# Kernel optimization log

Measured on AMD Instinct MI355X. Metric: run time of the kernel, lower is better.

## Reference

```python
import jax, jax.numpy as jnp
import numpy as np
from jax import lax

B, C, H, W, D = 2, 64, 32, 32, 32
N = H * W * D          # input_size = 32768
P = 64                 # proj_size
NH = 4                 # num_heads
HD = C // NH           # head dim = 16
LN_EPS = 1e-5
BN_EPS = 1e-5


def setup_inputs() -> dict:
    key = jax.random.key(0)
    ks = jax.random.split(key, 10)
    s = lambda k, shape: (jax.random.normal(k, shape, jnp.float32) * 0.02)
    return dict(
        x=jax.random.normal(ks[0], (B, C, H, W, D), jnp.float32),
        ln_w=jnp.ones((C,), jnp.float32), ln_b=jnp.zeros((C,), jnp.float32),
        gamma=1e-6 * jnp.ones((C,), jnp.float32),
        temp1=jnp.ones((NH, 1, 1), jnp.float32),
        temp2=jnp.ones((NH, 1, 1), jnp.float32),
        W_qkvv=s(ks[1], (4 * C, C)),                      # Linear(C,4C), no bias
        W_EF=s(ks[2], (P, N)), b_EF=jnp.zeros((P,), jnp.float32),  # shared E=F
        W_o1=s(ks[3], (C // 2, C)), b_o1=jnp.zeros((C // 2,), jnp.float32),
        W_o2=s(ks[4], (C // 2, C)), b_o2=jnp.zeros((C // 2,), jnp.float32),
        conv1_w=s(ks[5], (C, C, 3, 3, 3)),
        conv2_w=s(ks[6], (C, C, 3, 3, 3)),
        bn1_w=jnp.ones((C,), jnp.float32), bn1_b=jnp.zeros((C,), jnp.float32),
        bn2_w=jnp.ones((C,), jnp.float32), bn2_b=jnp.zeros((C,), jnp.float32),
        conv8_w=s(ks[7], (C, C, 1, 1, 1)), conv8_b=jnp.zeros((C,), jnp.float32),
    )


def _ln(x, w, b):
    mu = jnp.mean(x, axis=-1, keepdims=True)
    var = jnp.mean(jnp.square(x - mu), axis=-1, keepdims=True)
    return (x - mu) * lax.rsqrt(var + LN_EPS) * w + b


def _l2norm(x):  # F.normalize(dim=-1), eps=1e-12
    n = jnp.sqrt(jnp.sum(jnp.square(x), axis=-1, keepdims=True))
    return x / jnp.maximum(n, 1e-12)


def _bn_eval(x, w, b):  # BatchNorm3d in eval mode, running mean 0 / var 1
    scale = (w * lax.rsqrt(jnp.float32(1.0 + BN_EPS))).reshape(1, -1, 1, 1, 1)
    return x * scale + b.reshape(1, -1, 1, 1, 1)


def _conv3d(x, w, pad):
    return lax.conv_general_dilated(
        x, w, window_strides=(1, 1, 1), padding=[(pad, pad)] * 3,
        dimension_numbers=('NCDHW', 'OIDHW', 'NCDHW'))


def _lrelu(x):
    return jnp.where(x >= 0, x, 0.01 * x)


def _epa(xn, W_qkvv, W_EF, b_EF, temp1, temp2, W_o1, b_o1, W_o2, b_o2):
    b, n, c = xn.shape
    qkvv = (xn @ W_qkvv.T).reshape(b, n, 4, NH, HD).transpose(2, 0, 3, 1, 4)  # [4,B,h,N,d]
    q, k, v_ca, v_sa = [jnp.swapaxes(qkvv[i], -2, -1) for i in range(4)]      # [B,h,d,N]
    # shared linear projection E = F over the token axis N -> P
    k_proj = jnp.einsum('bhdn,pn->bhdp', k, W_EF) + b_EF
    v_proj = jnp.einsum('bhdn,pn->bhdp', v_sa, W_EF) + b_EF
    qn, kn = _l2norm(q), _l2norm(k)
    # channel attention: [B,h,d,d]
    attn_ca = jax.nn.softmax(jnp.einsum('bhdn,bhen->bhde', qn, kn) * temp1, axis=-1)
    x_ca = jnp.einsum('bhde,bhen->bhdn', attn_ca, v_ca)                       # [B,h,d,N]
    x_ca = x_ca.transpose(0, 3, 1, 2).reshape(b, n, c)
    # spatial attention with projected K/V: [B,h,N,P]
    attn_sa = jax.nn.softmax(jnp.einsum('bhdn,bhdp->bhnp', qn, k_proj) * temp2, axis=-1)
    x_sa = jnp.einsum('bhnp,bhdp->bhnd', attn_sa, v_proj)                     # [B,h,N,d]
    # faithful to original UNETR++ code: permute(0,3,1,2) then reshape(B,N,C)
    x_sa = x_sa.transpose(0, 3, 1, 2).reshape(b, n, c)
    x_sa = x_sa @ W_o1.T + b_o1
    x_ca = x_ca @ W_o2.T + b_o2
    return jnp.concatenate([x_sa, x_ca], axis=-1)


def reference(x, ln_w, ln_b, gamma, temp1, temp2, W_qkvv, W_EF, b_EF,
              W_o1, b_o1, W_o2, b_o2, conv1_w, conv2_w,
              bn1_w, bn1_b, bn2_w, bn2_b, conv8_w, conv8_b):
    b, c, h, w, d = x.shape
    xs = x.reshape(b, c, h * w * d).transpose(0, 2, 1)  # [B,N,C]
    attn = xs + gamma * _epa(_ln(xs, ln_w, ln_b), W_qkvv, W_EF, b_EF,
                             temp1, temp2, W_o1, b_o1, W_o2, b_o2)
    attn_skip = attn.reshape(b, h, w, d, c).transpose(0, 4, 1, 2, 3)  # [B,C,H,W,D]
    # UnetResBlock (stride 1, in==out -> identity residual), BN in eval mode
    out = _lrelu(_bn_eval(_conv3d(attn_skip, conv1_w, 1), bn1_w, bn1_b))
    out = _bn_eval(_conv3d(out, conv2_w, 1), bn2_w, bn2_b)
    out = _lrelu(out + attn_skip)
    # conv8: Dropout3d (off, eval) + 1x1x1 conv with bias
    y = _conv3d(out, conv8_w, 0) + conv8_b.reshape(1, -1, 1, 1, 1)
    return attn_skip + y
```

## Files before the change

kernel.cpp:

```cpp
#include <hip/hip_runtime.h>

#define NTOK 32768

typedef __attribute__((ext_vector_type(8))) short short8;
typedef __attribute__((ext_vector_type(4))) short short4_t;
typedef __attribute__((ext_vector_type(4))) float f32x4;

__device__ __forceinline__ short f2b(float f) {
    union { float f; unsigned u; } v; v.f = f;
    unsigned r = v.u + 0x7fffu + ((v.u >> 16) & 1u);
    return (short)(r >> 16);
}
__device__ __forceinline__ float b2f(short s) {
    union { float f; unsigned u; } v;
    v.u = ((unsigned)(unsigned short)s) << 16;
    return v.f;
}

__global__ void k_repack(const float* __restrict__ w1, const float* __restrict__ w2,
                         const float* __restrict__ w8, const float* __restrict__ wef,
                         const float* __restrict__ wq, const float* __restrict__ bEF,
                         short* __restrict__ wb1, short* __restrict__ wb2,
                         short* __restrict__ wb8, short* __restrict__ wefb,
                         short* __restrict__ wqb, float* __restrict__ kp,
                         float* __restrict__ vp, float* __restrict__ qd)
{
    int i = blockIdx.x * 256 + threadIdx.x;
    if (i >= 2349312) return;
    if (i >= 2347008) { qd[i - 2347008] = 0.f; return; }
    if (i >= 2338816) {
        int j = i - 2338816;
        float v = bEF[j & 63];
        kp[j] = v; vp[j] = v; return;
    }
    if (i >= 2322432) { int j = i - 2322432; wqb[j] = f2b(wq[j]); return; }
    if (i >= 225280)  { int j = i - 225280;  wefb[j] = f2b(wef[j]); return; }
    if (i >= 221184)  { int j = i - 221184;  wb8[j] = f2b(w8[j]); return; }
    int sel = i >= 110592;
    int j = sel ? i - 110592 : i;
    int tap = j >> 12;
    int r = j & 4095;
    int oc = r >> 6, ic = r & 63;
    const float* w = sel ? w2 : w1;
    short* o = sel ? wb2 : wb1;
    o[j] = f2b(w[(oc * 64 + ic) * 27 + tap]);
}

__global__ __launch_bounds__(256) void k_ln_qkvv(
    const float* __restrict__ x, const float* __restrict__ lnw,
    const float* __restrict__ lnb, const short* __restrict__ wqb,
    short* __restrict__ qkvvb)
{
    __shared__ __align__(16) short Wl[256 * 72];
    __shared__ __align__(16) short tr[256 * 72];
    __shared__ float red1[4][64], red2[4][64];
    __shared__ float mu_s[64], rs_s[64];
    short* al = tr;

    int bid = blockIdx.x;
    int b = bid >> 9;
    int n0 = (bid & 511) << 6;
    int tid = threadIdx.x;

    for (int i = tid; i < 2048; i += 256) {
        int out = i >> 3, q8 = (i & 7) * 8;
        *(short8*)&Wl[out * 72 + q8] = *(const short8*)&wqb[out * 64 + q8];
    }

    int t = tid & 63, cq = tid >> 6;
    float xr[16];
    float s1 = 0.f, s2 = 0.f;
    const float* xb = x + (((size_t)(b * 64 + cq * 16)) << 15) + n0 + t;
#pragma unroll
    for (int j = 0; j < 16; ++j) {
        float v = xb[(size_t)j << 15];
        xr[j] = v; s1 += v; s2 += v * v;
    }
    red1[cq][t] = s1; red2[cq][t] = s2;
    __syncthreads();
    if (tid < 64) {
        float a = red1[0][tid] + red1[1][tid] + red1[2][tid] + red1[3][tid];
        float q = red2[0][tid] + red2[1][tid] + red2[2][tid] + red2[3][tid];
        float mu = a * (1.f / 64.f);
        float var = q * (1.f / 64.f) - mu * mu;
        mu_s[tid] = mu;
        rs_s[tid] = rsqrtf(var + 1e-5f);
    }
    __syncthreads();
    {
        float mu = mu_s[t], rs = rs_s[t];
        short8 p0, p1;
#pragma unroll
        for (int j = 0; j < 8; ++j) {
            int c = cq * 16 + j;
            p0[j] = f2b((xr[j] - mu) * rs * lnw[c] + lnb[c]);
        }
#pragma unroll
        for (int j = 0; j < 8; ++j) {
            int c = cq * 16 + 8 + j;
            p1[j] = f2b((xr[8 + j] - mu) * rs * lnw[c] + lnb[c]);
        }
        *(short8*)&al[t * 72 + cq * 16] = p0;
        *(short8*)&al[t * 72 + cq * 16 + 8] = p1;
    }
    __syncthreads();

    int w = tid >> 6, lane = tid & 63, l15 = lane & 15, quad = lane >> 4;
    f32x4 acc[4][4];
#pragma unroll
    for (int mt = 0; mt < 4; ++mt)
#pragma unroll
        for (int nt = 0; nt < 4; ++nt) acc[mt][nt] = (f32x4){0.f, 0.f, 0.f, 0.f};
#pragma unroll
    for (int ks = 0; ks < 2; ++ks) {
        short8 af[4], bf[4];
#pragma unroll
        for (int mt = 0; mt < 4; ++mt)
            af[mt] = *(const short8*)&al[(mt * 16 + l15) * 72 + quad * 8 + ks * 32];
#pragma unroll
        for (int nt = 0; nt < 4; ++nt)
            bf[nt] = *(const short8*)&Wl[(w * 64 + nt * 16 + l15) * 72 + quad * 8 + ks * 32];
#pragma unroll
        for (int mt = 0; mt < 4; ++mt)
#pragma unroll
            for (int nt = 0; nt < 4; ++nt)
                acc[mt][nt] = __builtin_amdgcn_mfma_f32_16x16x32_bf16(af[mt], bf[nt], acc[mt][nt], 0, 0, 0);
    }
    __syncthreads();

#pragma unroll
    for (int mt = 0; mt < 4; ++mt)
#pragma unroll
        for (int nt = 0; nt < 4; ++nt) {
            int out = w * 64 + nt * 16 + l15;
            short4_t sv;
#pragma unroll
            for (int r = 0; r < 4; ++r) sv[r] = f2b(acc[mt][nt][r]);
            *(short4_t*)&tr[out * 72 + mt * 16 + quad * 4] = sv;
        }
    __syncthreads();
    for (int i = tid; i < 2048; i += 256) {
        int o = i >> 3, tq = (i & 7) * 8;
        short8 v = *(const short8*)&tr[o * 72 + tq];
        int isel = o >> 6, h = (o >> 4) & 3, d = o & 15;
        *(short8*)&qkvvb[((size_t)(((isel * 2 + b) * 4 + h) * 16 + d) << 15) + n0 + tq] = v;
    }
}

__global__ __launch_bounds__(256) void k_pq(
    const short* __restrict__ qkvvb, const short* __restrict__ wefb,
    float* __restrict__ kp, float* __restrict__ vp, float* __restrict__ qd,
    float* __restrict__ qn_acc, float* __restrict__ kn_acc)
{
    __shared__ float redb[3][64][38];
    int kc = blockIdx.x, bh = blockIdx.y;
    int tid = threadIdx.x;
    int w = tid >> 6, lane = tid & 63, l15 = lane & 15, quad = lane >> 4;
    size_t qrow = ((size_t)(bh * 16 + l15)) << 15;
    size_t krow = ((size_t)(128 + bh * 16 + l15)) << 15;
    size_t vrow = ((size_t)(384 + bh * 16 + l15)) << 15;
    int nbase = kc * 1024 + w * 256 + quad * 8;
    f32x4 acck[4], accv[4], accqd, accqq, acckk;
#pragma unroll
    for (int nt = 0; nt < 4; ++nt) {
        acck[nt] = (f32x4){0.f, 0.f, 0.f, 0.f};
        accv[nt] = (f32x4){0.f, 0.f, 0.f, 0.f};
    }
    accqd = (f32x4){0.f, 0.f, 0.f, 0.f};
    accqq = (f32x4){0.f, 0.f, 0.f, 0.f};
    acckk = (f32x4){0.f, 0.f, 0.f, 0.f};
#pragma unroll
    for (int ks = 0; ks < 8; ++ks) {
        int n = nbase + ks * 32;
        short8 qf = *(const short8*)&qkvvb[qrow + n];
        short8 kf = *(const short8*)&qkvvb[krow + n];
        short8 vf = *(const short8*)&qkvvb[vrow + n];
        accqd = __builtin_amdgcn_mfma_f32_16x16x32_bf16(qf, kf, accqd, 0, 0, 0);
        accqq = __builtin_amdgcn_mfma_f32_16x16x32_bf16(qf, qf, accqq, 0, 0, 0);
        acckk = __builtin_amdgcn_mfma_f32_16x16x32_bf16(kf, kf, acckk, 0, 0, 0);
#pragma unroll
        for (int nt = 0; nt < 4; ++nt) {
            short8 wf = *(const short8*)&wefb[(((size_t)(nt * 16 + l15)) << 15) + n];
            acck[nt] = __builtin_amdgcn_mfma_f32_16x16x32_bf16(kf, wf, acck[nt], 0, 0, 0);
            accv[nt] = __builtin_amdgcn_mfma_f32_16x16x32_bf16(vf, wf, accv[nt], 0, 0, 0);
        }
    }
    int diag = (quad == (l15 >> 2));
    float qqv = diag ? accqq[l15 & 3] : 0.f;
    float kkv = diag ? acckk[l15 & 3] : 0.f;
    if (w > 0) {
        float* p = &redb[w - 1][lane][0];
#pragma unroll
        for (int nt = 0; nt < 4; ++nt)
#pragma unroll
            for (int r = 0; r < 4; ++r) { p[nt * 4 + r] = acck[nt][r]; p[16 + nt * 4 + r] = accv[nt][r]; }
#pragma unroll
        for (int r = 0; r < 4; ++r) p[32 + r] = accqd[r];
        p[36] = qqv; p[37] = kkv;
    }
    __syncthreads();
    if (w == 0) {
#pragma unroll
        for (int wv = 0; wv < 3; ++wv) {
            const float* p = &redb[wv][lane][0];
#pragma unroll
            for (int nt = 0; nt < 4; ++nt)
#pragma unroll
                for (int r = 0; r < 4; ++r) { acck[nt][r] += p[nt * 4 + r]; accv[nt][r] += p[16 + nt * 4 + r]; }
#pragma unroll
            for (int r = 0; r < 4; ++r) accqd[r] += p[32 + r];
            qqv += p[36]; kkv += p[37];
        }
        int d = quad * 4;
#pragma unroll
        for (int nt = 0; nt < 4; ++nt)
#pragma unroll
            for (int r = 0; r < 4; ++r) {
                int idx = (bh * 16 + d + r) * 64 + nt * 16 + l15;
                atomicAdd(&kp[idx], acck[nt][r]);
                atomicAdd(&vp[idx], accv[nt][r]);
            }
#pragma unroll
        for (int r = 0; r < 4; ++r)
            atomicAdd(&qd[bh * 256 + (d + r) * 16 + l15], accqd[r]);
        if (diag) {
            atomicAdd(&qn_acc[bh * 16 + l15], qqv);
            atomicAdd(&kn_acc[bh * 16 + l15], kkv);
        }
    }
}

__global__ __launch_bounds__(256) void k_attn(
    const short* __restrict__ qkvvb, const float* __restrict__ qd,
    const float* __restrict__ qn_acc, const float* __restrict__ kn_acc,
    const float* __restrict__ temp1, const float* __restrict__ kp,
    const float* __restrict__ vp, const float* __restrict__ temp2,
    short* __restrict__ xsab, short* __restrict__ xcab)
{
    __shared__ float kl[16][68];
    __shared__ float vl[16][68];
    __shared__ float alca[16][17];
    __shared__ float iqs[16], iks[16];
    __shared__ __align__(16) short Pl[4][64][72];
    __shared__ short Ol[4][64][17];
    int bh = blockIdx.y; int b = bh >> 2, h = bh & 3;
    int tid = threadIdx.x;
    for (int i = tid; i < 1024; i += 256) {
        kl[i >> 6][i & 63] = kp[bh * 1024 + i];
        vl[i >> 6][i & 63] = vp[bh * 1024 + i];
    }
    if (tid < 32) {
        int j = tid & 15;
        float v = (tid < 16) ? qn_acc[bh * 16 + j] : kn_acc[bh * 16 + j];
        float rv = 1.f / fmaxf(sqrtf(v), 1e-12f);
        if (tid < 16) iqs[j] = rv; else iks[j] = rv;
    }
    __syncthreads();
    {
        int r = tid >> 4, e = tid & 15;
        float v = qd[bh * 256 + tid] * iqs[r] * iks[e] * temp1[h];
        float mx = v;
#pragma unroll
        for (int m = 1; m < 16; m <<= 1) mx = fmaxf(mx, __shfl_xor(mx, m));
        float ex = __expf(v - mx);
        float s = ex;
#pragma unroll
        for (int m = 1; m < 16; m <<= 1) s += __shfl_xor(s, m);
        alca[r][e] = ex / s;
    }
    __syncthreads();

    int w = tid >> 6, lane = tid & 63, l15 = lane & 15, quad = lane >> 4;
    int tw = (blockIdx.x << 8) + w * 64;
    float t2 = temp2[h];
    const short8 zero8 = {0, 0, 0, 0, 0, 0, 0, 0};
    int xs = (l15 & 7) << 3;

    short8 qb[4];
    if (quad < 2) {
#pragma unroll
        for (int tnt = 0; tnt < 4; ++tnt) {
            short8 v;
#pragma unroll
            for (int j = 0; j < 8; ++j) {
                int d = quad * 8 + j;
                short qv = qkvvb[(((size_t)(bh * 16 + d)) << 15) + tw + tnt * 16 + l15];
                v[j] = f2b(b2f(qv) * iqs[d]);
            }
            qb[tnt] = v;
        }
    } else {
#pragma unroll
        for (int tnt = 0; tnt < 4; ++tnt) qb[tnt] = zero8;
    }
    short8 ka[4];
    if (quad < 2) {
#pragma unroll
        for (int pmt = 0; pmt < 4; ++pmt) {
            short8 v;
#pragma unroll
            for (int j = 0; j < 8; ++j) v[j] = f2b(kl[quad * 8 + j][pmt * 16 + l15]);
            ka[pmt] = v;
        }
    } else {
#pragma unroll
        for (int pmt = 0; pmt < 4; ++pmt) ka[pmt] = zero8;
    }

    f32x4 st[4][4];
#pragma unroll
    for (int pmt = 0; pmt < 4; ++pmt)
#pragma unroll
        for (int tnt = 0; tnt < 4; ++tnt) st[pmt][tnt] = (f32x4){0.f, 0.f, 0.f, 0.f};
#pragma unroll
    for (int pmt = 0; pmt < 4; ++pmt)
#pragma unroll
        for (int tnt = 0; tnt < 4; ++tnt)
            st[pmt][tnt] = __builtin_amdgcn_mfma_f32_16x16x32_bf16(ka[pmt], qb[tnt], st[pmt][tnt], 0, 0, 0);

#pragma unroll
    for (int tnt = 0; tnt < 4; ++tnt) {
        int tok = tnt * 16 + l15;
        float v[16];
        float mx = -1e30f;
#pragma unroll
        for (int pmt = 0; pmt < 4; ++pmt)
#pragma unroll
            for (int r = 0; r < 4; ++r) {
                float x = st[pmt][tnt][r] * t2;
                v[pmt * 4 + r] = x; mx = fmaxf(mx, x);
            }
        mx = fmaxf(mx, __shfl_xor(mx, 16));
        mx = fmaxf(mx, __shfl_xor(mx, 32));
        float s = 0.f;
#pragma unroll
        for (int i2 = 0; i2 < 16; ++i2) { v[i2] = __expf(v[i2] - mx); s += v[i2]; }
        s += __shfl_xor(s, 16);
        s += __shfl_xor(s, 32);
        float inv = 1.f / s;
#pragma unroll
        for (int pmt = 0; pmt < 4; ++pmt)
#pragma unroll
            for (int t = 0; t < 2; ++t) {
                unsigned lo = (unsigned short)f2b(v[pmt * 4 + 2 * t] * inv);
                unsigned hi = (unsigned short)f2b(v[pmt * 4 + 2 * t + 1] * inv);
                int col = (pmt * 16 + quad * 4 + 2 * t) ^ xs;
                *(unsigned*)&Pl[w][tok][col] = lo | (hi << 16);
            }
    }

    short8 vb[2];
#pragma unroll
    for (int ks = 0; ks < 2; ++ks) {
        short8 t;
#pragma unroll
        for (int j = 0; j < 8; ++j) t[j] = f2b(vl[l15][quad * 8 + ks * 32 + j]);
        vb[ks] = t;
    }
    f32x4 vo[4];
#pragma unroll
    for (int mt = 0; mt < 4; ++mt) vo[mt] = (f32x4){0.f, 0.f, 0.f, 0.f};
#pragma unroll
    for (int mt = 0; mt < 4; ++mt) {
        int tok = mt * 16 + l15;
#pragma unroll
        for (int ks = 0; ks < 2; ++ks) {
            short8 pa = *(const short8*)&Pl[w][tok][(quad * 8 + ks * 32) ^ xs];
            vo[mt] = __builtin_amdgcn_mfma_f32_16x16x32_bf16(pa, vb[ks], vo[mt], 0, 0, 0);
        }
    }

    short8 ab[4], bb;
    if (quad < 2) {
        short8 t;
#pragma unroll
        for (int j = 0; j < 8; ++j) t[j] = f2b(alca[l15][quad * 8 + j]);
        bb = t;
#pragma unroll
        for (int mt = 0; mt < 4; ++mt) {
            short8 u;
#pragma unroll
            for (int j = 0; j < 8; ++j)
                u[j] = qkvvb[(((size_t)(256 + bh * 16 + quad * 8 + j)) << 15) + tw + mt * 16 + l15];
            ab[mt] = u;
        }
    } else {
        bb = zero8;
#pragma unroll
        for (int mt = 0; mt < 4; ++mt) ab[mt] = zero8;
    }
    f32x4 ca[4];
#pragma unroll
    for (int mt = 0; mt < 4; ++mt) ca[mt] = (f32x4){0.f, 0.f, 0.f, 0.f};
#pragma unroll
    for (int mt = 0; mt < 4; ++mt)
        ca[mt] = __builtin_amdgcn_mfma_f32_16x16x32_bf16(ab[mt], bb, ca[mt], 0, 0, 0);

#pragma unroll
    for (int mt = 0; mt < 4; ++mt)
#pragma unroll
        for (int r = 0; r < 4; ++r) {
            int tok = tw + mt * 16 + quad * 4 + r;
            xcab[((size_t)(b * NTOK + tok)) * 64 + h * 16 + l15] = f2b(ca[mt][r]);
        }

#pragma unroll
    for (int mt = 0; mt < 4; ++mt)
#pragma unroll
        for (int r = 0; r < 4; ++r)
            Ol[w][mt * 16 + quad * 4 + r][l15] = f2b(vo[mt][r]);
#pragma unroll
    for (int d = 0; d < 16; ++d) {
        short vv = Ol[w][lane][d];
        xsab[(size_t)b * 2097152 + (((size_t)(d * 4 + h)) << 15) + tw + lane] = vv;
    }
}

__global__ __launch_bounds__(256) void k_epilogue(
    const float* __restrict__ x, const short* __restrict__ xsab,
    const short* __restrict__ xcab, const float* __restrict__ Wo1,
    const float* __restrict__ bo1, const float* __restrict__ Wo2,
    const float* __restrict__ bo2, const float* __restrict__ gamma,
    float* __restrict__ attn_skip, short* __restrict__ gA)
{
    __shared__ __align__(16) short Wl[64 * 72];
    __shared__ __align__(16) short trS[256 * 72];
    int tid = threadIdx.x;
    int bidx = blockIdx.x;
    int b = bidx >> 7;
    int n0 = (bidx & 127) << 8;
    for (int i = tid; i < 4096; i += 256) {
        int row = i >> 6, c = i & 63;
        float wv = (row < 32) ? Wo1[row * 64 + c] : Wo2[(row - 32) * 64 + c];
        Wl[row * 72 + c] = f2b(wv);
    }
    __syncthreads();

    int w = tid >> 6, lane = tid & 63, l15 = lane & 15, quad = lane >> 4;
    int tw = n0 + w * 64;
    const short* sa_base = xsab + (size_t)b * 2097152;
    const short* ca_base = xcab + (size_t)b * 2097152;

    f32x4 acc_sa[4][2], acc_ca[4][2];
#pragma unroll
    for (int mt = 0; mt < 4; ++mt)
#pragma unroll
        for (int nt = 0; nt < 2; ++nt) {
            acc_sa[mt][nt] = (f32x4){0.f, 0.f, 0.f, 0.f};
            acc_ca[mt][nt] = (f32x4){0.f, 0.f, 0.f, 0.f};
        }
#pragma unroll
    for (int ks = 0; ks < 2; ++ks) {
        int ko = quad * 8 + ks * 32;
        short8 b1[2], b2[2];
#pragma unroll
        for (int nt = 0; nt < 2; ++nt) {
            b1[nt] = *(const short8*)&Wl[(nt * 16 + l15) * 72 + ko];
            b2[nt] = *(const short8*)&Wl[(32 + nt * 16 + l15) * 72 + ko];
        }
#pragma unroll
        for (int mt = 0; mt < 4; ++mt) {
            int trow = tw + mt * 16 + l15;
            short8 a1 = *(const short8*)&sa_base[(size_t)trow * 64 + ko];
            short8 a2 = *(const short8*)&ca_base[(size_t)trow * 64 + ko];
#pragma unroll
            for (int nt = 0; nt < 2; ++nt) {
                acc_sa[mt][nt] = __builtin_amdgcn_mfma_f32_16x16x32_bf16(a1, b1[nt], acc_sa[mt][nt], 0, 0, 0);
                acc_ca[mt][nt] = __builtin_amdgcn_mfma_f32_16x16x32_bf16(a2, b2[nt], acc_ca[mt][nt], 0, 0, 0);
            }
        }
    }

#pragma unroll
    for (int half = 0; half < 2; ++half) {
#pragma unroll
        for (int nt = 0; nt < 2; ++nt) {
            int c = half * 32 + nt * 16 + l15;
            float g = gamma[c];
            float bias = half ? bo2[c - 32] : bo1[c];
#pragma unroll
            for (int mt = 0; mt < 4; ++mt) {
                f32x4 a = half ? acc_ca[mt][nt] : acc_sa[mt][nt];
                int tbase = tw + mt * 16 + quad * 4;
                size_t gidx = (((size_t)(b * 64 + c)) << 15) + tbase;
                f32x4 xv = *(const f32x4*)&x[gidx];
                f32x4 o;
#pragma unroll
                for (int r = 0; r < 4; ++r) {
                    float v = xv[r] + g * (a[r] + bias);
                    o[r] = v;
                    trS[(w * 64 + mt * 16 + quad * 4 + r) * 72 + c] = f2b(v);
                }
                *(f32x4*)&attn_skip[gidx] = o;
            }
        }
    }
    __syncthreads();
    for (int i = tid; i < 2048; i += 256) {
        int tok = i >> 3, cq = (i & 7) * 8;
        short8 v = *(const short8*)&trS[tok * 72 + cq];
        *(short8*)&gA[((size_t)(b * NTOK + n0 + tok)) * 64 + cq] = v;
    }
}

template <int MODE>
__global__ __launch_bounds__(256) void k_conv3m(
    const short* __restrict__ gin, const short* __restrict__ wb,
    const float* __restrict__ bnw, const float* __restrict__ bnb,
    const float* __restrict__ skip, short* __restrict__ goutS,
    const short* __restrict__ wb8, const float* __restrict__ b8,
    float* __restrict__ io)
{
    __shared__ __align__(16) short inl_s[24480];
    __shared__ __align__(16) short wl_s[15360];
    int bx = blockIdx.x;
    int bb = bx >> 8;
    int z0 = (bx >> 3) & 31;
    int y0 = (bx & 7) * 4;
    int tid = threadIdx.x;
    int lane = tid & 63, wv = tid >> 6;
    int l15 = lane & 15, quad = lane >> 4;
    int wo = tid >> 2, wq = tid & 3;

    f32x4 acc[2][4];
#pragma unroll
    for (int s = 0; s < 2; ++s)
#pragma unroll
        for (int nt = 0; nt < 4; ++nt) acc[s][nt] = (f32x4){0.f, 0.f, 0.f, 0.f};

    for (int chunk = 0; chunk < 2; ++chunk) {
        const short* wck = wb + chunk * 32 + wq * 8;
        short8 wr[3];
#pragma unroll
        for (int t = 0; t < 3; ++t)
            wr[t] = *(const short8*)&wck[(size_t)(t * 64 + wo) * 64];
        __syncthreads();
        for (int i = tid; i < 2448; i += 256) {
            int p = i >> 2, icq = i & 3;
            int xi = p % 34; int t2 = p / 34; int yi = t2 % 6; int zi = t2 / 6;
            int gz = z0 + zi - 1, gy = y0 + yi - 1, gx = xi - 1;
            short8 v = {0, 0, 0, 0, 0, 0, 0, 0};
            if ((unsigned)gz < 32u && (unsigned)gy < 32u && (unsigned)gx < 32u)
                v = *(const short8*)&gin[((size_t)(bb * NTOK + gz * 1024 + gy * 32 + gx)) * 64 + chunk * 32 + icq * 8];
            *(short8*)&inl_s[p * 40 + icq * 8] = v;
        }
#pragma unroll
        for (int t = 0; t < 3; ++t)
            *(short8*)&wl_s[(t * 64 + wo) * 40 + wq * 8] = wr[t];

#pragma unroll
        for (int kz = 0; kz < 3; ++kz)
#pragma unroll
        for (int ky = 0; ky < 3; ++ky) {
            const int sidx = kz * 3 + ky;
            __syncthreads();
            if (sidx < 8) {
#pragma unroll
                for (int t = 0; t < 3; ++t)
                    wr[t] = *(const short8*)&wck[(size_t)(((sidx + 1) * 3 + t) * 64 + wo) * 64];
            }
            const short* wcur = &wl_s[(sidx & 1) * 7680];
            int rowb = (kz * 6 + wv + ky) * 34;
#pragma unroll
            for (int kx = 0; kx < 3; ++kx) {
                short8 bf[4];
#pragma unroll
                for (int nt = 0; nt < 4; ++nt)
                    bf[nt] = *(const short8*)&wcur[(kx * 64 + nt * 16 + l15) * 40 + quad * 8];
#pragma unroll
                for (int s = 0; s < 2; ++s) {
                    short8 af = *(const short8*)&inl_s[(rowb + s * 16 + l15 + kx) * 40 + quad * 8];
#pragma unroll
                    for (int nt = 0; nt < 4; ++nt)
                        acc[s][nt] = __builtin_amdgcn_mfma_f32_16x16x32_bf16(af, bf[nt], acc[s][nt], 0, 0, 0);
                }
            }
            if (sidx < 8) {
                short* wnext = &wl_s[((sidx + 1) & 1) * 7680];
#pragma unroll
                for (int t = 0; t < 3; ++t)
                    *(short8*)&wnext[(t * 64 + wo) * 40 + wq * 8] = wr[t];
            }
        }
    }
    __syncthreads();
    float rb = rsqrtf(1.f + 1e-5f);
    if (MODE == 0) {
        short* outS = inl_s;
#pragma unroll
        for (int nt = 0; nt < 4; ++nt) {
            int oc = nt * 16 + l15;
            float sc_ = bnw[oc] * rb, sh_ = bnb[oc];
#pragma unroll
            for (int s = 0; s < 2; ++s) {
                f32x4 v = acc[s][nt];
#pragma unroll
                for (int r = 0; r < 4; ++r) {
                    int pos = wv * 32 + s * 16 + quad * 4 + r;
                    float val = v[r] * sc_ + sh_;
                    val = val >= 0.f ? val : 0.01f * val;
                    outS[pos * 72 + oc] = f2b(val);
                }
            }
        }
        __syncthreads();
        for (int i = tid; i < 1024; i += 256) {
            int p = i >> 3, cq = i & 7;
            short8 v = *(const short8*)&outS[p * 72 + cq * 8];
            int y = p >> 5, x = p & 31;
            *(short8*)&goutS[((size_t)(bb * NTOK + z0 * 1024 + (y0 + y) * 32 + x)) * 64 + cq * 8] = v;
        }
    } else {
        float* outF = (float*)inl_s;
        short* a2_s = wl_s;
        short* w8_s = wl_s + 9216;
#pragma unroll
        for (int nt = 0; nt < 4; ++nt) {
            int oc = nt * 16 + l15;
#pragma unroll
            for (int s = 0; s < 2; ++s) {
                f32x4 v = acc[s][nt];
#pragma unroll
                for (int r = 0; r < 4; ++r) {
                    int pos = wv * 32 + s * 16 + quad * 4 + r;
                    outF[oc * 132 + pos] = v[r];
                }
            }
        }
        __syncthreads();
        f32x4 skr[8];
#pragma unroll
        for (int it = 0; it < 8; ++it) {
            int i = it * 256 + tid;
            int oc = i >> 5, xq = i & 31, pos0 = xq * 4;
            f32x4 c4 = *(const f32x4*)&outF[oc * 132 + pos0];
            int y = pos0 >> 5, xx = pos0 & 31;
            size_t g = (((size_t)(bb * 64 + oc)) << 15) + ((z0 * 32 + (y0 + y)) * 32 + xx);
            f32x4 sk = *(const f32x4*)&skip[g];
            skr[it] = sk;
            float sc_ = bnw[oc] * rb, sh_ = bnb[oc];
#pragma unroll
            for (int r = 0; r < 4; ++r) {
                float val = c4[r] * sc_ + sh_ + sk[r];
                val = val >= 0.f ? val : 0.01f * val;
                a2_s[(pos0 + r) * 72 + oc] = f2b(val);
            }
        }
        for (int i = tid; i < 512; i += 256) {
            int ocw = i >> 3, cq = i & 7;
            *(short8*)&w8_s[ocw * 80 + cq * 8] = *(const short8*)&wb8[ocw * 64 + cq * 8];
        }
        __syncthreads();
        f32x4 acc2[2][4];
#pragma unroll
        for (int s = 0; s < 2; ++s)
#pragma unroll
            for (int nt = 0; nt < 4; ++nt) acc2[s][nt] = (f32x4){0.f, 0.f, 0.f, 0.f};
#pragma unroll
        for (int ks = 0; ks < 2; ++ks) {
            short8 a8[2], b8f[4];
#pragma unroll
            for (int s = 0; s < 2; ++s)
                a8[s] = *(const short8*)&a2_s[(wv * 32 + s * 16 + l15) * 72 + quad * 8 + ks * 32];
#pragma unroll
            for (int nt = 0; nt < 4; ++nt)
                b8f[nt] = *(const short8*)&w8_s[(nt * 16 + l15) * 80 + quad * 8 + ks * 32];
#pragma unroll
            for (int s = 0; s < 2; ++s)
#pragma unroll
                for (int nt = 0; nt < 4; ++nt)
                    acc2[s][nt] = __builtin_amdgcn_mfma_f32_16x16x32_bf16(a8[s], b8f[nt], acc2[s][nt], 0, 0, 0);
        }
        __syncthreads();
#pragma unroll
        for (int nt = 0; nt < 4; ++nt) {
            int oc = nt * 16 + l15;
#pragma unroll
            for (int s = 0; s < 2; ++s) {
                f32x4 v = acc2[s][nt];
#pragma unroll
                for (int r = 0; r < 4; ++r) {
                    int pos = wv * 32 + s * 16 + quad * 4 + r;
                    outF[oc * 132 + pos] = v[r];
                }
            }
        }
        __syncthreads();
#pragma unroll
        for (int it = 0; it < 8; ++it) {
            int i = it * 256 + tid;
            int oc = i >> 5, xq = i & 31, pos0 = xq * 4;
            f32x4 cv = *(const f32x4*)&outF[oc * 132 + pos0];
            int y = pos0 >> 5, xx = pos0 & 31;
            size_t g = (((size_t)(bb * 64 + oc)) << 15) + ((z0 * 32 + (y0 + y)) * 32 + xx);
            float bias8 = b8[oc];
            f32x4 o;
#pragma unroll
            for (int r = 0; r < 4; ++r) o[r] = skr[it][r] + cv[r] + bias8;
            *(f32x4*)&io[g] = o;
        }
    }
}

extern "C" void kernel_launch(void* const* d_in, const int* in_sizes, int n_in,
                              void* d_out, int out_size, void* d_ws, size_t ws_size,
                              hipStream_t stream) {
    const float* x      = (const float*)d_in[0];
    const float* ln_w   = (const float*)d_in[1];
    const float* ln_b   = (const float*)d_in[2];
    const float* gamma  = (const float*)d_in[3];
    const float* temp1  = (const float*)d_in[4];
    const float* temp2  = (const float*)d_in[5];
    const float* W_qkvv = (const float*)d_in[6];
    const float* W_EF   = (const float*)d_in[7];
    const float* b_EF   = (const float*)d_in[8];
    const float* W_o1   = (const float*)d_in[9];
    const float* b_o1   = (const float*)d_in[10];
    const float* W_o2   = (const float*)d_in[11];
    const float* b_o2   = (const float*)d_in[12];
    const float* conv1w = (const float*)d_in[13];
    const float* conv2w = (const float*)d_in[14];
    const float* bn1_w  = (const float*)d_in[15];
    const float* bn1_b  = (const float*)d_in[16];
    const float* bn2_w  = (const float*)d_in[17];
    const float* bn2_b  = (const float*)d_in[18];
    const float* conv8w = (const float*)d_in[19];
    const float* conv8b = (const float*)d_in[20];

    short* qkvvb = (short*)d_ws;
    float* kp    = (float*)(qkvvb + 16777216);
    float* vp    = kp + 8192;
    float* qd    = vp + 8192;
    float* qn_acc= qd + 2048;
    float* kn_acc= qn_acc + 128;
    float* a_ca  = kn_acc + 128;
    float* iqn   = a_ca + 2048;
    float* ikn   = iqn + 128;
    short* xcab  = (short*)(ikn + 128);
    short* xsab  = xcab + 4194304;
    short* gA    = xsab + 4194304;
    short* g1    = gA + 4194304;
    short* wb1   = g1 + 4194304;
    short* wb2   = wb1 + 110592;
    short* wb8   = wb2 + 110592;
    short* wefb  = wb8 + 4096;
    short* wqb   = wefb + 2097152;

    float* attn_skip = (float*)d_out;

    hipLaunchKernelGGL(k_repack, dim3(9177), dim3(256), 0, stream,
                       conv1w, conv2w, conv8w, W_EF, W_qkvv, b_EF,
                       wb1, wb2, wb8, wefb, wqb, kp, vp, qd);
    hipLaunchKernelGGL(k_ln_qkvv, dim3(1024), dim3(256), 0, stream,
                       x, ln_w, ln_b, wqb, qkvvb);
    hipLaunchKernelGGL(k_pq, dim3(32, 8), dim3(256), 0, stream,
                       qkvvb, wefb, kp, vp, qd, qn_acc, kn_acc);
    hipLaunchKernelGGL(k_attn, dim3(128, 8), dim3(256), 0, stream,
                       qkvvb, qd, qn_acc, kn_acc, temp1, kp, vp, temp2, xsab, xcab);
    hipLaunchKernelGGL(k_epilogue, dim3(256), dim3(256), 0, stream,
                       x, xsab, xcab, W_o1, b_o1, W_o2, b_o2, gamma, attn_skip, gA);
    hipLaunchKernelGGL((k_conv3m<0>), dim3(512), dim3(256), 0, stream,
                       gA, wb1, bn1_w, bn1_b, (const float*)nullptr, g1,
                       (const short*)nullptr, (const float*)nullptr, (float*)nullptr);
    hipLaunchKernelGGL((k_conv3m<1>), dim3(512), dim3(256), 0, stream,
                       g1, wb2, bn2_w, bn2_b, attn_skip, (short*)nullptr,
                       wb8, conv8b, attn_skip);
}
```

Baseline: 218.2 us.

## Prefetch conv weights two stages ahead and drop LDS round-trips in conv2 epilogue

Weight prefetch for the 3x3x3 conv now uses two register buffers, loading the slice two kz/ky stages ahead so global latency has more time to hide. In the MODE 1 epilogue, the conv2 accumulators are combined with the skip tensor directly from the MFMA output layout. The final 1x1x1 conv result is also written straight to global memory, which removes the fp32 LDS transpose staging and two barriers. The cost is more VGPRs, and the global reads and writes become less coalesced (16-byte pieces per lane rather than contiguous rows).

```diff
diff --git a/kernel.cpp b/kernel.cpp
--- a/kernel.cpp
+++ b/kernel.cpp
@@ -530,10 +530,12 @@
 
     for (int chunk = 0; chunk < 2; ++chunk) {
         const short* wck = wb + chunk * 32 + wq * 8;
-        short8 wr[3];
-#pragma unroll
-        for (int t = 0; t < 3; ++t)
-            wr[t] = *(const short8*)&wck[(size_t)(t * 64 + wo) * 64];
+        short8 wr[2][3];
+#pragma unroll
+        for (int t = 0; t < 3; ++t) {
+            wr[0][t] = *(const short8*)&wck[(size_t)(t * 64 + wo) * 64];
+            wr[1][t] = *(const short8*)&wck[(size_t)((3 + t) * 64 + wo) * 64];
+        }
         __syncthreads();
         for (int i = tid; i < 2448; i += 256) {
             int p = i >> 2, icq = i & 3;
@@ -546,7 +548,7 @@
         }
 #pragma unroll
         for (int t = 0; t < 3; ++t)
-            *(short8*)&wl_s[(t * 64 + wo) * 40 + wq * 8] = wr[t];
+            *(short8*)&wl_s[(t * 64 + wo) * 40 + wq * 8] = wr[0][t];
 
 #pragma unroll
         for (int kz = 0; kz < 3; ++kz)
@@ -554,10 +556,10 @@
         for (int ky = 0; ky < 3; ++ky) {
             const int sidx = kz * 3 + ky;
             __syncthreads();
-            if (sidx < 8) {
+            if (sidx < 7) {
 #pragma unroll
                 for (int t = 0; t < 3; ++t)
-                    wr[t] = *(const short8*)&wck[(size_t)(((sidx + 1) * 3 + t) * 64 + wo) * 64];
+                    wr[sidx & 1][t] = *(const short8*)&wck[(size_t)(((sidx + 2) * 3 + t) * 64 + wo) * 64];
             }
             const short* wcur = &wl_s[(sidx & 1) * 7680];
             int rowb = (kz * 6 + wv + ky) * 34;
@@ -579,7 +581,7 @@
                 short* wnext = &wl_s[((sidx + 1) & 1) * 7680];
 #pragma unroll
                 for (int t = 0; t < 3; ++t)
-                    *(short8*)&wnext[(t * 64 + wo) * 40 + wq * 8] = wr[t];
+                    *(short8*)&wnext[(t * 64 + wo) * 40 + wq * 8] = wr[(sidx + 1) & 1][t];
             }
         }
     }
@@ -611,39 +613,27 @@
             *(short8*)&goutS[((size_t)(bb * NTOK + z0 * 1024 + (y0 + y) * 32 + x)) * 64 + cq * 8] = v;
         }
     } else {
-        float* outF = (float*)inl_s;
         short* a2_s = wl_s;
         short* w8_s = wl_s + 9216;
+        f32x4 skr[2][4];
 #pragma unroll
         for (int nt = 0; nt < 4; ++nt) {
             int oc = nt * 16 + l15;
+            float sc_ = bnw[oc] * rb, sh_ = bnb[oc];
 #pragma unroll
             for (int s = 0; s < 2; ++s) {
+                size_t g = (((size_t)(bb * 64 + oc)) << 15) +
+                           ((z0 * 32 + y0 + wv) * 32 + s * 16 + quad * 4);
+                f32x4 sk = *(const f32x4*)&skip[g];
+                skr[s][nt] = sk;
                 f32x4 v = acc[s][nt];
 #pragma unroll
                 for (int r = 0; r < 4; ++r) {
                     int pos = wv * 32 + s * 16 + quad * 4 + r;
-                    outF[oc * 132 + pos] = v[r];
+                    float val = v[r] * sc_ + sh_ + sk[r];
+                    val = val >= 0.f ? val : 0.01f * val;
+                    a2_s[pos * 72 + oc] = f2b(val);
                 }
-            }
-        }
-        __syncthreads();
-        f32x4 skr[8];
-#pragma unroll
-        for (int it = 0; it < 8; ++it) {
-            int i = it * 256 + tid;
-            int oc = i >> 5, xq = i & 31, pos0 = xq * 4;
-            f32x4 c4 = *(const f32x4*)&outF[oc * 132 + pos0];
-            int y = pos0 >> 5, xx = pos0 & 31;
-            size_t g = (((size_t)(bb * 64 + oc)) << 15) + ((z0 * 32 + (y0 + y)) * 32 + xx);
-            f32x4 sk = *(const f32x4*)&skip[g];
-            skr[it] = sk;
-            float sc_ = bnw[oc] * rb, sh_ = bnb[oc];
-#pragma unroll
-            for (int r = 0; r < 4; ++r) {
-                float val = c4[r] * sc_ + sh_ + sk[r];
-                val = val >= 0.f ? val : 0.01f * val;
-                a2_s[(pos0 + r) * 72 + oc] = f2b(val);
             }
         }
         for (int i = tid; i < 512; i += 256) {
@@ -671,33 +661,19 @@
                 for (int nt = 0; nt < 4; ++nt)
                     acc2[s][nt] = __builtin_amdgcn_mfma_f32_16x16x32_bf16(a8[s], b8f[nt], acc2[s][nt], 0, 0, 0);
         }
-        __syncthreads();
 #pragma unroll
         for (int nt = 0; nt < 4; ++nt) {
             int oc = nt * 16 + l15;
+            float bias8 = b8[oc];
 #pragma unroll
             for (int s = 0; s < 2; ++s) {
-                f32x4 v = acc2[s][nt];
-#pragma unroll
-                for (int r = 0; r < 4; ++r) {
-                    int pos = wv * 32 + s * 16 + quad * 4 + r;
-                    outF[oc * 132 + pos] = v[r];
-                }
-            }
-        }
-        __syncthreads();
-#pragma unroll
-        for (int it = 0; it < 8; ++it) {
-            int i = it * 256 + tid;
-            int oc = i >> 5, xq = i & 31, pos0 = xq * 4;
-            f32x4 cv = *(const f32x4*)&outF[oc * 132 + pos0];
-            int y = pos0 >> 5, xx = pos0 & 31;
-            size_t g = (((size_t)(bb * 64 + oc)) << 15) + ((z0 * 32 + (y0 + y)) * 32 + xx);
-            float bias8 = b8[oc];
-            f32x4 o;
-#pragma unroll
-            for (int r = 0; r < 4; ++r) o[r] = skr[it][r] + cv[r] + bias8;
-            *(f32x4*)&io[g] = o;
+                size_t g = (((size_t)(bb * 64 + oc)) << 15) +
+                           ((z0 * 32 + y0 + wv) * 32 + s * 16 + quad * 4);
+                f32x4 o;
+#pragma unroll
+                for (int r = 0; r < 4; ++r) o[r] = skr[s][nt][r] + acc2[s][nt][r] + bias8;
+                *(f32x4*)&io[g] = o;
+            }
         }
     }
 }
```

New measurement: 216.2 us. Within noise of the previous version (-0.9%).
